# Optimization experiments

Measured on AMD Instinct MI355X. Metric: run time of the kernel, lower is better.

## Reference

```python
import jax, jax.numpy as jnp
import numpy as np
import math

MAX_L = 8                       # spherical-harmonic max degree
R = 0.95                        # poincare disk radius
ENERGY_THR = 0.9999
GOLDEN = 0.618033988749
LM = [(l, m) for l in range(MAX_L + 1) for m in range(-l, l + 1)]  # 81 pairs


def _assoc_legendre(x, l, m):
    # m >= 0, standard upward recurrence; x is a vector
    if l == 0 and m == 0:
        return jnp.ones_like(x)
    pmm = jnp.ones_like(x)
    if m > 0:
        somx2 = jnp.sqrt(1.0 - x * x)
        fact = 1.0
        for _ in range(m):
            pmm = pmm * (-fact * somx2)
            fact += 2.0
    if l == m:
        return pmm
    pmmp1 = x * (2 * m + 1) * pmm
    if l == m + 1:
        return pmmp1
    pll, plp1 = pmm, pmmp1
    for ll in range(m + 2, l + 1):
        pnew = ((2 * ll - 1) * x * plp1 - (ll + m - 1) * pll) / (ll - m)
        pll, plp1 = plp1, pnew
    return plp1


def _harmonic(cos_t, phi, l, m):
    P = _assoc_legendre(cos_t, l, abs(m))
    norm = math.sqrt((2 * l + 1) * math.factorial(l - abs(m))
                     / math.factorial(l + abs(m)) / (4.0 * math.pi))
    ang = jnp.cos(m * phi) if m >= 0 else jnp.sin(abs(m) * phi)
    return norm * P * ang


def _sphere_coords(zr, zi):
    # hyperbolic radius -> polar angle on sphere; phi = complex argument
    r = jnp.sqrt(zr * zr + zi * zi)
    phi = jnp.arctan2(zi, zr)
    cos_t = jnp.cos(2.0 * jnp.arctanh(jnp.minimum(r, 0.99)) * math.pi / (2.0 * MAX_L))
    return cos_t, phi


def _forward_transform(w):
    flat = w.reshape(-1)
    if flat.shape[0] % 2 == 1:
        flat = jnp.concatenate([flat, jnp.zeros((1,), flat.dtype)])
    re, im = flat[0::2], flat[1::2]
    mag = jnp.sqrt(re * re + im * im)
    scale = jnp.max(mag)
    safe = jnp.where(scale > 0, scale, 1.0)
    a, b = re / safe, im / safe
    # complex tanh(a+ib) = (sinh 2a + i sin 2b) / (cosh 2a + cos 2b)
    den = jnp.cosh(2 * a) + jnp.cos(2 * b)
    pr = jnp.where(scale > 0, jnp.sinh(2 * a) / den * R, re)
    pi_ = jnp.where(scale > 0, jnp.sin(2 * b) / den * R, im)
    cos_t, phi = _sphere_coords(pr, pi_)
    coeffs = jnp.stack([jnp.mean(_harmonic(cos_t, phi, l, m)) for l, m in LM])
    return coeffs, scale, re.shape[0]


def _compress(c):
    # adaptive top-energy masking (decompress restores zeros -> masking is exact)
    n = c.shape[0]
    mag = jnp.abs(c)
    order = jnp.argsort(-mag)
    e = jnp.cumsum(mag[order] ** 2)
    tot = e[-1]
    kc = jnp.where(tot > 0,
                   jnp.sum(e / jnp.maximum(tot, 1e-30) <= ENERGY_THR) + 1,
                   n)
    kc = jnp.maximum(kc, n // 2)
    ranks = jnp.zeros((n,), jnp.int32).at[order].set(jnp.arange(n, dtype=jnp.int32))
    return jnp.where(ranks < kc, c, 0.0)


def _inverse_transform(c, scale, num_points, shape):
    i = jnp.arange(num_points, dtype=jnp.float32)
    r = jnp.minimum((i + 0.5) / num_points * R, 0.95)
    theta = jnp.mod(2.0 * math.pi * i * GOLDEN, 1.0)
    zr, zi = r * jnp.cos(theta), r * jnp.sin(theta)
    cos_t, phi = _sphere_coords(zr, zi)
    cm = jnp.where(jnp.abs(c) > 1e-10, c, 0.0)
    recon = jnp.zeros((num_points,), jnp.float32)
    for idx, (l, m) in enumerate(LM):
        recon = recon + cm[idx] * _harmonic(cos_t, phi, l, m)
    real = jnp.where(scale > 0, recon * scale, recon)
    # interleave (real, imag=0) as in torch stack([re, im], 1).flatten()
    flat = jnp.stack([real, jnp.zeros_like(real)], axis=1).reshape(-1)
    total = int(np.prod(shape))
    if flat.shape[0] > total:
        flat = flat[:total]
    elif flat.shape[0] < total:
        flat = jnp.concatenate([flat, jnp.zeros((total - flat.shape[0],), flat.dtype)])
    return flat.reshape(shape)


def setup_inputs() -> dict:
    key = jax.random.key(0)
    ks = jax.random.split(key, 5)
    return {
        "x": jax.random.normal(ks[0], (8, 1024, 768), jnp.float32),
        "w_fc": jax.random.normal(ks[1], (2, 3072, 768), jnp.float32) * 0.02,
        "w_proj": jax.random.normal(ks[2], (2, 768, 3072), jnp.float32) * 0.02,
        "b_fc": jax.random.normal(ks[3], (2, 3072), jnp.float32) * 0.02,
        "b_proj": jax.random.normal(ks[4], (2, 768), jnp.float32) * 0.02,
    }


def reference(x, w_fc, w_proj, b_fc, b_proj):
    L = w_fc.shape[0]
    imp = jax.nn.softmax(jnp.arange(L, dtype=jnp.float32) * 0.5)
    fused_fc = jnp.einsum('l,lij->ij', imp, w_fc)
    fused_proj = jnp.einsum('l,lij->ij', imp, w_proj)
    bias_fc = jnp.einsum('l,li->i', imp, b_fc)
    bias_proj = jnp.einsum('l,li->i', imp, b_proj)

    c_fc, s_fc, n_fc = _forward_transform(fused_fc)
    W_fc = _inverse_transform(_compress(c_fc), s_fc, n_fc, fused_fc.shape)
    c_pr, s_pr, n_pr = _forward_transform(fused_proj)
    W_proj = _inverse_transform(_compress(c_pr), s_pr, n_pr, fused_proj.shape)

    h = jax.nn.gelu(jnp.einsum('bsd,fd->bsf', x, W_fc) + bias_fc, approximate=False)
    return jnp.einsum('bsf,df->bsd', h, W_proj) + bias_proj
```

## Files before the change

### kernel.cpp

```cpp
#include <hip/hip_runtime.h>

#define MAXL 8
#define NC 81
#define NPAIR 1179648
#define TOTW  2359296
#define PI_F 3.14159265358979323846f
#define CO_BLOCKS 256

typedef __attribute__((ext_vector_type(8))) __bf16 bf16x8;
typedef __attribute__((ext_vector_type(4))) float f32x4;
typedef __attribute__((address_space(3))) void lds_void;
typedef const __attribute__((address_space(1))) void glb_void;

constexpr double cfact(int n){ double r=1.0; for(int i=2;i<=n;++i) r*=(double)i; return r; }
constexpr double csqrtd(double x){
  double r = (x > 1.0) ? x : 1.0;
  for (int i=0;i<200;++i) r = 0.5*(r + x/r);
  return r;
}
struct Norms { float v[NC]; };
constexpr Norms make_norms(){
  Norms t{};
  for (int l=0;l<=MAXL;++l)
    for (int m=-l;m<=l;++m){
      int am = m<0?-m:m;
      double nn = csqrtd((double)(2*l+1)*cfact(l-am)/cfact(l+am)/(4.0*3.14159265358979323846));
      t.v[l*l+l+m] = (float)nn;
    }
  return t;
}
__constant__ Norms g_norm = make_norms();

__device__ __forceinline__ float fast_atanh(float x){
  return 0.5f * __logf((1.0f + x) * __builtin_amdgcn_rcpf(1.0f - x));
}

__global__ __launch_bounds__(256) void k_max(const float* __restrict__ wfc,
    const float* __restrict__ wpr, int* __restrict__ scaleBits,
    double* __restrict__ gacc, float imp0, float imp1){
  const int mat = blockIdx.y;
  if (mat == 0 && blockIdx.x == 0 && threadIdx.x < 2*NC) gacc[threadIdx.x] = 0.0;
  const float2* w0 = (const float2*)(mat ? wpr : wfc);
  const float2* w1 = w0 + (TOTW/2);
  float vmax = 0.0f;
  for (int i = blockIdx.x*blockDim.x + threadIdx.x; i < NPAIR; i += gridDim.x*blockDim.x){
    float2 a = w0[i], b = w1[i];
    float re = fmaf(imp0, a.x, imp1*b.x);
    float im = fmaf(imp0, a.y, imp1*b.y);
    vmax = fmaxf(vmax, sqrtf(re*re + im*im));
  }
  for (int off=32; off; off>>=1) vmax = fmaxf(vmax, __shfl_down(vmax, off));
  __shared__ float red[4];
  int lane = threadIdx.x & 63, wv = threadIdx.x >> 6;
  if (lane == 0) red[wv] = vmax;
  __syncthreads();
  if (threadIdx.x == 0){
    float m = fmaxf(fmaxf(red[0], red[1]), fmaxf(red[2], red[3]));
    atomicMax(scaleBits + mat, (int)__float_as_uint(m));
  }
}

__global__ __launch_bounds__(256,2) void k_coeff(const float* __restrict__ wfc,
                                                 const float* __restrict__ wpr,
                                                 const unsigned* __restrict__ scaleBits,
                                                 double* __restrict__ gacc){
  const int mat = blockIdx.y;
  const float2* w0 = (const float2*)(mat ? wpr : wfc);
  const float2* w1 = w0 + (TOTW/2);
  const float scale = __uint_as_float(scaleBits[mat]);
  const bool has = scale > 0.0f;
  const float inv_safe = 1.0f / (has ? scale : 1.0f);
  const float imp0 = (float)0.37754066879814546;
  const float imp1 = (float)0.62245933120185454;

  float acc[NC];
  #pragma unroll
  for (int v=0; v<NC; ++v) acc[v] = 0.0f;

  auto map1 = [&](int idx, float& X, float& c1, float& s1, float& st){
    float2 av = w0[idx], bv = w1[idx];
    float re = fmaf(imp0, av.x, imp1*bv.x);
    float im = fmaf(imp0, av.y, imp1*bv.y);
    float pr, pi_;
    if (has){
      float a = re*inv_safe, b = im*inv_safe;
      float e  = __expf(2.0f*a);
      float ie = __builtin_amdgcn_rcpf(e);
      float ch = 0.5f*(e + ie), sh = 0.5f*(e - ie);
      float s2b, c2b; __sincosf(2.0f*b, &s2b, &c2b);
      float inv_den = __builtin_amdgcn_rcpf(ch + c2b);
      pr  = sh*inv_den*0.95f;
      pi_ = s2b*inv_den*0.95f;
    } else { pr = re; pi_ = im; }
    float r2 = pr*pr + pi_*pi_;
    float inv_r = (r2 > 0.0f) ? __builtin_amdgcn_rsqf(r2) : 0.0f;
    c1 = (r2 > 0.0f) ? pr*inv_r : 1.0f;
    s1 = pi_*inv_r;
    float rr_ = r2*inv_r;
    float arg = fast_atanh(fminf(rr_, 0.99f)) * (PI_F/8.0f);
    __sincosf(arg, &st, &X);
  };

  const int T = CO_BLOCKS*256;
  for (int i = blockIdx.x*blockDim.x + threadIdx.x; i < NPAIR/2; i += T){
    float X0,c10,s10,st0, X1,c11,s11,st1;
    map1(i,           X0, c10, s10, st0);
    map1(i + NPAIR/2, X1, c11, s11, st1);

    float cm0=1.0f, sm0=0.0f, pm0=1.0f;
    float cm1=1.0f, sm1=0.0f, pm1=1.0f;
    float fact=1.0f;
    #pragma unroll
    for (int m=0; m<=MAXL; ++m){
      if (m > 0){
        float t0 = cm0*c10 - sm0*s10; sm0 = sm0*c10 + cm0*s10; cm0 = t0;
        float t1 = cm1*c11 - sm1*s11; sm1 = sm1*c11 + cm1*s11; cm1 = t1;
        pm0 = pm0 * (-fact*st0);
        pm1 = pm1 * (-fact*st1);
        fact += 2.0f;
      }
      float a1 = pm0, b1 = pm1;
      acc[m*m + 2*m] += a1*cm0 + b1*cm1;
      if (m > 0) acc[m*m] += a1*sm0 + b1*sm1;
      if (m < MAXL){
        float a0 = a1, b0 = b1;
        a1 = X0*(float)(2*m+1)*a0;
        b1 = X1*(float)(2*m+1)*b0;
        acc[(m+1)*(m+1) + (m+1) + m] += a1*cm0 + b1*cm1;
        if (m > 0) acc[(m+1)*(m+1) + 1] += a1*sm0 + b1*sm1;
        #pragma unroll
        for (int l=m+2; l<=MAXL; ++l){
          float an = ((float)(2*l-1)*X0*a1 - (float)(l+m-1)*a0) * (1.0f/(float)(l-m));
          a0 = a1; a1 = an;
          float bn = ((float)(2*l-1)*X1*b1 - (float)(l+m-1)*b0) * (1.0f/(float)(l-m));
          b0 = b1; b1 = bn;
          acc[l*l + l + m] += a1*cm0 + b1*cm1;
          if (m > 0) acc[l*l + l - m] += a1*sm0 + b1*sm1;
        }
      }
    }
  }

  __shared__ float redf[4][NC];
  int lane = threadIdx.x & 63, wv = threadIdx.x >> 6;
  #pragma unroll
  for (int v=0; v<NC; ++v){
    float d = acc[v];
    for (int off=32; off; off>>=1) d += __shfl_down(d, off);
    if (lane == 0) redf[wv][v] = d;
  }
  __syncthreads();
  for (int v = threadIdx.x; v < NC; v += blockDim.x){
    double s = (double)redf[0][v] + (double)redf[1][v] + (double)redf[2][v] + (double)redf[3][v];
    unsafeAtomicAdd(gacc + mat*NC + v, s);
  }
}

__global__ __launch_bounds__(128) void k_compress(const double* __restrict__ gacc,
                                                  float* __restrict__ cfin){
  const int mat = blockIdx.x;
  const int v = threadIdx.x;
  __shared__ float mg[NC];
  __shared__ float smg2[NC];
  __shared__ int cnt_sh;

  float c = 0.0f, m = -1.0f;
  if (v < NC){
    double m_ = (double)g_norm.v[v] * gacc[mat*NC + v] / (double)NPAIR;
    c = (float)m_;
    m = fabsf(c);
    mg[v] = m;
  }
  if (v == 0) cnt_sh = 0;
  __syncthreads();

  int rank = 0;
  if (v < NC){
    #pragma unroll 1
    for (int u = 0; u < NC; ++u){
      float mu = mg[u];
      rank += (mu > m) || (mu == m && u < v);
    }
    smg2[rank] = m*m;
  }
  __syncthreads();

  float e_mine = 0.0f, tot = 0.0f;
  if (v < NC){
    float run = 0.0f;
    #pragma unroll 1
    for (int u = 0; u < NC; ++u){
      run += smg2[u];
      if (u == rank) e_mine = run;
    }
    tot = run;
    float den = fmaxf(tot, 1e-30f);
    if (tot > 0.0f && (e_mine / den <= 0.9999f)) atomicAdd(&cnt_sh, 1);
  }
  __syncthreads();

  if (v < NC){
    int kc = (tot > 0.0f) ? (cnt_sh + 1) : NC;
    if (kc < NC/2) kc = NC/2;
    float cv = (rank < kc) ? c : 0.0f;
    if (fabsf(cv) <= 1e-10f) cv = 0.0f;
    cfin[mat*NC + v] = cv;
  }
}

__global__ __launch_bounds__(256) void k_inverse(const float* __restrict__ cfin,
    const unsigned* __restrict__ scaleBits, __bf16* __restrict__ B1, __bf16* __restrict__ B2,
    const float* __restrict__ x, __bf16* __restrict__ A1){
  __shared__ float cA[NC], cB[NC], sc[2];
  if (threadIdx.x < NC){ cA[threadIdx.x] = cfin[threadIdx.x]; cB[threadIdx.x] = cfin[NC + threadIdx.x]; }
  if (threadIdx.x < 2) sc[threadIdx.x] = __uint_as_float(scaleBits[threadIdx.x]);
  __syncthreads();
  const int gid = blockIdx.x*blockDim.x + threadIdx.x;

  for (int t = gid; t < 8192*384; t += 4608*256){
    float2 v = ((const float2*)x)[t];
    A1[t] = (__bf16)v.x;
  }

  int j = gid;
  if (j >= NPAIR) return;

  float jf = (float)j;
  float r = fminf((jf + 0.5f) / 1179648.0f * 0.95f, 0.95f);
  float theta = fmodf((6.28318530717958647692f * jf) * 0.618033988749f, 1.0f);
  float phi = theta;
  float X, sint;
  {
    float arg = fast_atanh(fminf(r, 0.99f)) * (PI_F/8.0f);
    __sincosf(arg, &sint, &X);
  }
  float s1, c1; __sincosf(phi, &s1, &c1);

  float ra = 0.0f, rb = 0.0f;
  float cm = 1.0f, sm = 0.0f, pmm = 1.0f, fact = 1.0f;

  auto emit = [&](int l, int m, float P){
    int ip = l*l + l + m;
    float y = g_norm.v[ip] * P;
    float yc = y*cm;
    ra += cA[ip]*yc; rb += cB[ip]*yc;
    if (m > 0){
      int in_ = l*l + l - m;
      float ys = y*sm;
      ra += cA[in_]*ys; rb += cB[in_]*ys;
    }
  };

  #pragma unroll
  for (int m=0; m<=MAXL; ++m){
    if (m > 0){
      float t = cm*c1 - sm*s1;
      sm = sm*c1 + cm*s1;
      cm = t;
      pmm = pmm * (-fact*sint);
      fact += 2.0f;
    }
    float p0 = pmm;
    emit(m, m, p0);
    if (m < MAXL){
      float p1 = X*(float)(2*m+1)*p0;
      emit(m+1, m, p1);
      #pragma unroll
      for (int l=m+2; l<=MAXL; ++l){
        float pn = ((float)(2*l-1)*X*p1 - (float)(l+m-1)*p0) * (1.0f/(float)(l-m));
        p0 = p1; p1 = pn;
        emit(l, m, p1);
      }
    }
  }

  float sA = sc[0], sB = sc[1];
  B2[j] = (__bf16)((sB > 0.0f) ? rb*sB : rb);
  int q = j / 768, rem = j - q*768;
  if (rem < 384)
    B1[q*384 + rem] = (__bf16)((sA > 0.0f) ? ra*sA : ra);
}

template<int ACT, int OUTBF, int MI, int NJ>
__global__ __launch_bounds__(256) void k_gemm_mfma(
    const __bf16* __restrict__ A, const __bf16* __restrict__ B,
    const float* __restrict__ bias, int bmul, int blen,
    float imp0, float imp1,
    __bf16* __restrict__ Hout, float* __restrict__ Fout,
    int N, int K)
{
  constexpr int BM = 2*MI*16, BN = 2*NJ*16;
  constexpr int ACH = BM/16, NCH = (BM+BN)/16;
  static_assert(NCH % 4 == 0, "chunks must split across 4 waves");
  __shared__ __bf16 As[2][BM*32];
  __shared__ __bf16 Bs[2][BN*32];
  const int tid  = threadIdx.x;
  const int wave = tid >> 6, lane = tid & 63;
  const int wr = wave >> 1, wc = wave & 1;
  const int rr = lane & 15, kq = lane >> 4;
  const int sx = rr & 3;
  const int bm = blockIdx.y * BM, bn = blockIdx.x * BN;

  const int lrow  = lane >> 2;
  const int lslot = lane & 3;
  const int sslot = lslot ^ (lrow & 3);
  const __bf16* Abase = A + (size_t)bm * K;
  const __bf16* Bbase = B + (size_t)bn * K;

  f32x4 acc[MI][NJ] = {};

  auto stage = [&](int buf, int k0){
    #pragma unroll
    for (int is = 0; is < NCH/4; ++is) {
      const int c = is * 4 + wave;
      if (c < ACH) {
        const __bf16* ga = Abase + (size_t)(c*16 + lrow) * K + (k0 + sslot*8);
        __builtin_amdgcn_global_load_lds((glb_void*)ga, (lds_void*)(&As[buf][c*512]), 16, 0, 0);
      } else {
        const int cb = c - ACH;
        const __bf16* gb = Bbase + (size_t)(cb*16 + lrow) * K + (k0 + sslot*8);
        __builtin_amdgcn_global_load_lds((glb_void*)gb, (lds_void*)(&Bs[buf][cb*512]), 16, 0, 0);
      }
    }
  };

  const int nt = K/32;
  stage(0, 0);
  __syncthreads();

  for (int t = 0; t < nt; ++t) {
    const int cur = t & 1;
    if (t + 1 < nt) stage(cur ^ 1, (t+1)*32);

    bf16x8 af[MI], bfr[NJ];
    #pragma unroll
    for (int i=0;i<MI;++i){
      const int row = wr*MI*16 + i*16 + rr;
      af[i]  = *(const bf16x8*)&As[cur][row*32 + ((kq ^ sx) << 3)];
    }
    #pragma unroll
    for (int j=0;j<NJ;++j){
      const int row = wc*NJ*16 + j*16 + rr;
      bfr[j] = *(const bf16x8*)&Bs[cur][row*32 + ((kq ^ sx) << 3)];
    }
    #pragma unroll
    for (int i=0;i<MI;++i)
      #pragma unroll
      for (int j=0;j<NJ;++j)
        acc[i][j] = __builtin_amdgcn_mfma_f32_16x16x32_bf16(af[i], bfr[j], acc[i][j], 0, 0, 0);

    __syncthreads();
  }

  #pragma unroll
  for (int j=0;j<NJ;++j){
    const int col = bn + wc*NJ*16 + j*16 + rr;
    const float bb = imp0*bias[bmul*col] + imp1*bias[blen + bmul*col];
    #pragma unroll
    for (int i=0;i<MI;++i){
      const int row0 = bm + wr*MI*16 + i*16 + kq*4;
      #pragma unroll
      for (int t=0;t<4;++t){
        float v = acc[i][j][t] + bb;
        if (ACT) v = 0.5f*v*(1.0f + erff(v*0.70710678118654752440f));
        if (OUTBF) Hout[(size_t)(row0+t)*N + col] = (__bf16)v;
        else       Fout[(size_t)(row0+t)*N + col] = v;
      }
    }
  }
}

extern "C" void kernel_launch(void* const* d_in, const int* in_sizes, int n_in,
                              void* d_out, int out_size, void* d_ws, size_t ws_size,
                              hipStream_t stream){
  const float* x   = (const float*)d_in[0];
  const float* wfc = (const float*)d_in[1];
  const float* wpr = (const float*)d_in[2];
  const float* bfc = (const float*)d_in[3];
  const float* bpr = (const float*)d_in[4];
  float* out = (float*)d_out;

  char* ws = (char*)d_ws;
  size_t off = 0;
  auto alloc = [&](size_t bytes){ void* p = ws + off; off = (off + bytes + 255) & ~(size_t)255; return p; };

  unsigned* scaleBits= (unsigned*)alloc(8);
  double* gacc       = (double*)  alloc(2*NC*sizeof(double));
  float* cfin        = (float*)   alloc(2*NC*sizeof(float));
  __bf16* B1         = (__bf16*)  alloc((size_t)1536*384*sizeof(__bf16));
  __bf16* B2         = (__bf16*)  alloc((size_t)768*1536*sizeof(__bf16));
  __bf16* A1         = (__bf16*)  alloc((size_t)8192*384*sizeof(__bf16));
  __bf16* H          = (__bf16*)  alloc((size_t)8192*1536*sizeof(__bf16));

  const float imp0 = (float)0.37754066879814546;
  const float imp1 = (float)0.62245933120185454;

  k_max<<<dim3(256,2),256,0,stream>>>(wfc, wpr, (int*)scaleBits, gacc, imp0, imp1);
  k_coeff<<<dim3(CO_BLOCKS,2),256,0,stream>>>(wfc, wpr, scaleBits, gacc);
  k_compress<<<2,128,0,stream>>>(gacc, cfin);
  k_inverse<<<4608,256,0,stream>>>(cfin, scaleBits, B1, B2, x, A1);
  k_gemm_mfma<1,1,4,4><<<dim3(12,64),256,0,stream>>>(A1, B1, bfc, 2, 3072, imp0, imp1, H, nullptr, 1536, 384);
  k_gemm_mfma<0,0,4,4><<<dim3(6,64),256,0,stream>>>(H, B2, bpr, 1, 768, imp0, imp1, nullptr, out, 768, 1536);
}
```

Before: 166.4 us.

## Fold norms and scales into packed coeffs, two points per thread, XCD-swizzle GEMM grid

The compress step now runs both matrices in one block. It folds the per-harmonic norm and the weight scale into the coefficients and packs them as 45 float4 entries in (m,l) emission order. The inverse kernel reads these packed entries and evaluates two weight pairs per thread on half as many blocks, which removes the per-term norm multiplies and the separate cos/sin coefficient lookups. The GEMMs switch to a 1D grid whose block index is remapped in groups of 8, likely to spread neighbouring tiles across the chiplets for cache locality. In exchange the inverse kernel holds more live registers, and the remap assumes the grid size is divisible by 8.

```diff
diff --git a/kernel.cpp b/kernel.cpp
--- a/kernel.cpp
+++ b/kernel.cpp
@@ -2,10 +2,12 @@
 
 #define MAXL 8
 #define NC 81
+#define NE 45
 #define NPAIR 1179648
 #define TOTW  2359296
 #define PI_F 3.14159265358979323846f
 #define CO_BLOCKS 256
+#define INV_BLOCKS 2304
 
 typedef __attribute__((ext_vector_type(8))) __bf16 bf16x8;
 typedef __attribute__((ext_vector_type(4))) float f32x4;
@@ -30,6 +32,14 @@
   return t;
 }
 __constant__ Norms g_norm = make_norms();
+
+struct EmitML { unsigned char m[NE], l[NE]; };
+constexpr EmitML make_emit(){
+  EmitML e{}; int k=0;
+  for (int m=0;m<=MAXL;++m) for (int l=m;l<=MAXL;++l){ e.m[k]=(unsigned char)m; e.l[k]=(unsigned char)l; ++k; }
+  return e;
+}
+__constant__ EmitML g_emit = make_emit();
 
 __device__ __forceinline__ float fast_atanh(float x){
   return 0.5f * __logf((1.0f + x) * __builtin_amdgcn_rcpf(1.0f - x));
@@ -156,32 +166,34 @@
   }
 }
 
-__global__ __launch_bounds__(128) void k_compress(const double* __restrict__ gacc,
-                                                  float* __restrict__ cfin){
-  const int mat = blockIdx.x;
-  const int v = threadIdx.x;
-  __shared__ float mg[NC];
-  __shared__ float smg2[NC];
-  __shared__ int cnt_sh;
+__global__ __launch_bounds__(256) void k_compress(const double* __restrict__ gacc,
+    const unsigned* __restrict__ scaleBits, float4* __restrict__ eAB){
+  __shared__ float cf[2][NC];
+  __shared__ float mg[2][NC];
+  __shared__ float smg2[2][NC];
+  __shared__ int cnt_sh[2];
+  const int half = threadIdx.x >> 7;
+  const int v = threadIdx.x & 127;
+  if (threadIdx.x < 2) cnt_sh[threadIdx.x] = 0;
+  __syncthreads();
 
   float c = 0.0f, m = -1.0f;
   if (v < NC){
-    double m_ = (double)g_norm.v[v] * gacc[mat*NC + v] / (double)NPAIR;
+    double m_ = (double)g_norm.v[v] * gacc[half*NC + v] / (double)NPAIR;
     c = (float)m_;
     m = fabsf(c);
-    mg[v] = m;
-  }
-  if (v == 0) cnt_sh = 0;
+    mg[half][v] = m;
+  }
   __syncthreads();
 
   int rank = 0;
   if (v < NC){
     #pragma unroll 1
     for (int u = 0; u < NC; ++u){
-      float mu = mg[u];
+      float mu = mg[half][u];
       rank += (mu > m) || (mu == m && u < v);
     }
-    smg2[rank] = m*m;
+    smg2[half][rank] = m*m;
   }
   __syncthreads();
 
@@ -190,98 +202,120 @@
     float run = 0.0f;
     #pragma unroll 1
     for (int u = 0; u < NC; ++u){
-      run += smg2[u];
+      run += smg2[half][u];
       if (u == rank) e_mine = run;
     }
     tot = run;
     float den = fmaxf(tot, 1e-30f);
-    if (tot > 0.0f && (e_mine / den <= 0.9999f)) atomicAdd(&cnt_sh, 1);
+    if (tot > 0.0f && (e_mine / den <= 0.9999f)) atomicAdd(&cnt_sh[half], 1);
   }
   __syncthreads();
 
   if (v < NC){
-    int kc = (tot > 0.0f) ? (cnt_sh + 1) : NC;
+    int kc = (tot > 0.0f) ? (cnt_sh[half] + 1) : NC;
     if (kc < NC/2) kc = NC/2;
     float cv = (rank < kc) ? c : 0.0f;
     if (fabsf(cv) <= 1e-10f) cv = 0.0f;
-    cfin[mat*NC + v] = cv;
-  }
-}
-
-__global__ __launch_bounds__(256) void k_inverse(const float* __restrict__ cfin,
-    const unsigned* __restrict__ scaleBits, __bf16* __restrict__ B1, __bf16* __restrict__ B2,
+    float sc = __uint_as_float(scaleBits[half]);
+    float fold = (sc > 0.0f) ? sc : 1.0f;
+    cf[half][v] = cv * g_norm.v[v] * fold;
+  }
+  __syncthreads();
+
+  if (threadIdx.x < NE){
+    int mm = g_emit.m[threadIdx.x], ll = g_emit.l[threadIdx.x];
+    int ip = ll*ll + ll + mm, in_ = ll*ll + ll - mm;
+    float4 q;
+    q.x = cf[0][ip]; q.y = (mm > 0) ? cf[0][in_] : 0.0f;
+    q.z = cf[1][ip]; q.w = (mm > 0) ? cf[1][in_] : 0.0f;
+    eAB[threadIdx.x] = q;
+  }
+}
+
+__global__ __launch_bounds__(256) void k_inverse(const float4* __restrict__ eAB,
+    __bf16* __restrict__ B1, __bf16* __restrict__ B2,
     const float* __restrict__ x, __bf16* __restrict__ A1){
-  __shared__ float cA[NC], cB[NC], sc[2];
-  if (threadIdx.x < NC){ cA[threadIdx.x] = cfin[threadIdx.x]; cB[threadIdx.x] = cfin[NC + threadIdx.x]; }
-  if (threadIdx.x < 2) sc[threadIdx.x] = __uint_as_float(scaleBits[threadIdx.x]);
+  __shared__ float4 qs[NE];
+  if (threadIdx.x < NE) qs[threadIdx.x] = eAB[threadIdx.x];
   __syncthreads();
   const int gid = blockIdx.x*blockDim.x + threadIdx.x;
 
-  for (int t = gid; t < 8192*384; t += 4608*256){
+  for (int t = gid; t < 8192*384; t += INV_BLOCKS*256){
     float2 v = ((const float2*)x)[t];
     A1[t] = (__bf16)v.x;
   }
 
-  int j = gid;
-  if (j >= NPAIR) return;
-
-  float jf = (float)j;
-  float r = fminf((jf + 0.5f) / 1179648.0f * 0.95f, 0.95f);
-  float theta = fmodf((6.28318530717958647692f * jf) * 0.618033988749f, 1.0f);
-  float phi = theta;
-  float X, sint;
+  const int j0 = gid, j1 = gid + NPAIR/2;
+  float X0,s10,c10,st0, X1,s11,c11,st1;
   {
+    float jf = (float)j0;
+    float r = fminf((jf + 0.5f) / 1179648.0f * 0.95f, 0.95f);
+    float phi = fmodf((6.28318530717958647692f * jf) * 0.618033988749f, 1.0f);
     float arg = fast_atanh(fminf(r, 0.99f)) * (PI_F/8.0f);
-    __sincosf(arg, &sint, &X);
-  }
-  float s1, c1; __sincosf(phi, &s1, &c1);
-
-  float ra = 0.0f, rb = 0.0f;
-  float cm = 1.0f, sm = 0.0f, pmm = 1.0f, fact = 1.0f;
-
-  auto emit = [&](int l, int m, float P){
-    int ip = l*l + l + m;
-    float y = g_norm.v[ip] * P;
-    float yc = y*cm;
-    ra += cA[ip]*yc; rb += cB[ip]*yc;
-    if (m > 0){
-      int in_ = l*l + l - m;
-      float ys = y*sm;
-      ra += cA[in_]*ys; rb += cB[in_]*ys;
-    }
+    __sincosf(arg, &st0, &X0);
+    __sincosf(phi, &s10, &c10);
+  }
+  {
+    float jf = (float)j1;
+    float r = fminf((jf + 0.5f) / 1179648.0f * 0.95f, 0.95f);
+    float phi = fmodf((6.28318530717958647692f * jf) * 0.618033988749f, 1.0f);
+    float arg = fast_atanh(fminf(r, 0.99f)) * (PI_F/8.0f);
+    __sincosf(arg, &st1, &X1);
+    __sincosf(phi, &s11, &c11);
+  }
+
+  float ra0=0.0f, rb0=0.0f, ra1=0.0f, rb1=0.0f;
+  float cm0=1.0f, sm0=0.0f, pm0=1.0f;
+  float cm1=1.0f, sm1=0.0f, pm1=1.0f;
+  float fact=1.0f;
+  int k=0;
+
+  auto emit2 = [&](float Pa, float Pb){
+    float4 q = qs[k]; ++k;
+    float yc0 = Pa*cm0, ys0 = Pa*sm0;
+    float yc1 = Pb*cm1, ys1 = Pb*sm1;
+    ra0 += q.x*yc0; ra0 += q.y*ys0;
+    rb0 += q.z*yc0; rb0 += q.w*ys0;
+    ra1 += q.x*yc1; ra1 += q.y*ys1;
+    rb1 += q.z*yc1; rb1 += q.w*ys1;
   };
 
   #pragma unroll
   for (int m=0; m<=MAXL; ++m){
     if (m > 0){
-      float t = cm*c1 - sm*s1;
-      sm = sm*c1 + cm*s1;
-      cm = t;
-      pmm = pmm * (-fact*sint);
+      float t0 = cm0*c10 - sm0*s10; sm0 = sm0*c10 + cm0*s10; cm0 = t0;
+      float t1 = cm1*c11 - sm1*s11; sm1 = sm1*c11 + cm1*s11; cm1 = t1;
+      pm0 = pm0 * (-fact*st0);
+      pm1 = pm1 * (-fact*st1);
       fact += 2.0f;
     }
-    float p0 = pmm;
-    emit(m, m, p0);
+    float a1v = pm0, b1v = pm1;
+    emit2(a1v, b1v);
     if (m < MAXL){
-      float p1 = X*(float)(2*m+1)*p0;
-      emit(m+1, m, p1);
+      float a0v = a1v, b0v = b1v;
+      a1v = X0*(float)(2*m+1)*a0v;
+      b1v = X1*(float)(2*m+1)*b0v;
+      emit2(a1v, b1v);
       #pragma unroll
       for (int l=m+2; l<=MAXL; ++l){
-        float pn = ((float)(2*l-1)*X*p1 - (float)(l+m-1)*p0) * (1.0f/(float)(l-m));
-        p0 = p1; p1 = pn;
-        emit(l, m, p1);
+        float an = ((float)(2*l-1)*X0*a1v - (float)(l+m-1)*a0v) * (1.0f/(float)(l-m));
+        a0v = a1v; a1v = an;
+        float bn = ((float)(2*l-1)*X1*b1v - (float)(l+m-1)*b0v) * (1.0f/(float)(l-m));
+        b0v = b1v; b1v = bn;
+        emit2(a1v, b1v);
       }
     }
   }
 
-  float sA = sc[0], sB = sc[1];
-  B2[j] = (__bf16)((sB > 0.0f) ? rb*sB : rb);
-  int q = j / 768, rem = j - q*768;
-  if (rem < 384)
-    B1[q*384 + rem] = (__bf16)((sA > 0.0f) ? ra*sA : ra);
-}
-
-template<int ACT, int OUTBF, int MI, int NJ>
+  B2[j0] = (__bf16)rb0;
+  B2[j1] = (__bf16)rb1;
+  int q0 = j0 / 768, r0 = j0 - q0*768;
+  if (r0 < 384) B1[q0*384 + r0] = (__bf16)ra0;
+  int q1 = j1 / 768, r1 = j1 - q1*768;
+  if (r1 < 384) B1[q1*384 + r1] = (__bf16)ra1;
+}
+
+template<int ACT, int OUTBF, int MI, int NJ, int NBX>
 __global__ __launch_bounds__(256) void k_gemm_mfma(
     const __bf16* __restrict__ A, const __bf16* __restrict__ B,
     const float* __restrict__ bias, int bmul, int blen,
@@ -299,7 +333,10 @@
   const int wr = wave >> 1, wc = wave & 1;
   const int rr = lane & 15, kq = lane >> 4;
   const int sx = rr & 3;
-  const int bm = blockIdx.y * BM, bn = blockIdx.x * BN;
+
+  const int nwg = gridDim.x;
+  const int sb  = (blockIdx.x & 7)*(nwg >> 3) + (blockIdx.x >> 3);
+  const int bm = (sb / NBX) * BM, bn = (sb % NBX) * BN;
 
   const int lrow  = lane >> 2;
   const int lslot = lane & 3;
@@ -386,7 +423,7 @@
 
   unsigned* scaleBits= (unsigned*)alloc(8);
   double* gacc       = (double*)  alloc(2*NC*sizeof(double));
-  float* cfin        = (float*)   alloc(2*NC*sizeof(float));
+  float4* eAB        = (float4*)  alloc(NE*sizeof(float4));
   __bf16* B1         = (__bf16*)  alloc((size_t)1536*384*sizeof(__bf16));
   __bf16* B2         = (__bf16*)  alloc((size_t)768*1536*sizeof(__bf16));
   __bf16* A1         = (__bf16*)  alloc((size_t)8192*384*sizeof(__bf16));
@@ -397,8 +434,8 @@
 
   k_max<<<dim3(256,2),256,0,stream>>>(wfc, wpr, (int*)scaleBits, gacc, imp0, imp1);
   k_coeff<<<dim3(CO_BLOCKS,2),256,0,stream>>>(wfc, wpr, scaleBits, gacc);
-  k_compress<<<2,128,0,stream>>>(gacc, cfin);
-  k_inverse<<<4608,256,0,stream>>>(cfin, scaleBits, B1, B2, x, A1);
-  k_gemm_mfma<1,1,4,4><<<dim3(12,64),256,0,stream>>>(A1, B1, bfc, 2, 3072, imp0, imp1, H, nullptr, 1536, 384);
-  k_gemm_mfma<0,0,4,4><<<dim3(6,64),256,0,stream>>>(H, B2, bpr, 1, 768, imp0, imp1, nullptr, out, 768, 1536);
-}
+  k_compress<<<1,256,0,stream>>>(gacc, scaleBits, eAB);
+  k_inverse<<<INV_BLOCKS,256,0,stream>>>(eAB, B1, B2, x, A1);
+  k_gemm_mfma<1,1,4,4,12><<<768,256,0,stream>>>(A1, B1, bfc, 2, 3072, imp0, imp1, H, nullptr, 1536, 384);
+  k_gemm_mfma<0,0,4,4,6><<<384,256,0,stream>>>(H, B2, bpr, 1, 768, imp0, imp1, nullptr, out, 768, 1536);
+}
```

Result: slower. 171.9 us (+3.3%).
